# Kernel tuning notes

Measured on AMD Instinct MI355X. Metric: run time of the kernel, lower is better.

Reference implementation:

```python
import jax, jax.numpy as jnp
import numpy as np

B, T, D = 2, 2048, 2048
H, HD = 16, 128            # num_heads, head_dim = D // H
DVH = 2                    # dynamic_value_num_heads
NVK = 4                    # num_v_keys = int(sqrt(H))
TOPK = DVH * 2             # = 4 <= NVK


def setup_inputs() -> dict:
    key = jax.random.key(0)
    ks = jax.random.split(key, 12)
    s = jnp.float32(0.02)
    return {
        "x": jax.random.normal(ks[0], (B, T, D), jnp.float32),
        "Wq": jax.random.normal(ks[1], (D, D), jnp.float32) * s,
        "bq": jnp.zeros((D,), jnp.float32),
        "Wk": jax.random.normal(ks[2], (D, D), jnp.float32) * s,
        "bk": jnp.zeros((D,), jnp.float32),
        "Wvq": jax.random.normal(ks[3], (HD * DVH, D), jnp.float32) * s,
        "bvq": jnp.zeros((HD * DVH,), jnp.float32),
        "v_keys": jax.random.normal(ks[4], (DVH, NVK, HD), jnp.float32) * s,
        "v_embed": jax.random.normal(ks[5], (H, HD * H), jnp.float32) * s,
        "Wo": jax.random.normal(ks[6], (D, D), jnp.float32) * s,
        "bo": jnp.zeros((D,), jnp.float32),
    }


def reference(x, Wq, bq, Wk, bk, Wvq, bvq, v_keys, v_embed, Wo, bo):
    b, t, d = x.shape
    # q/k projections -> [b, H, t, HD]
    q = (x @ Wq.T + bq).reshape(b, t, H, HD).transpose(0, 2, 1, 3)
    k = (x @ Wk.T + bk).reshape(b, t, H, HD).transpose(0, 2, 1, 3)

    # --- compute_value_states ---
    vq = (x @ Wvq.T + bvq).reshape(b, t, DVH, HD)          # [b,t,h,n]
    sim = jnp.einsum('bthn,hkn->bthk', vq, v_keys)         # [b,t,DVH,NVK]
    _, idx = jax.lax.top_k(sim, TOPK)                      # [b,t,DVH,TOPK]
    ve = v_embed[idx]                                      # gather -> [b,t,DVH,TOPK,d]
    # einsum 'btd,bthkd->btd' == x * sum over (h,k)
    vs = x * ve.sum(axis=(2, 3))                           # [b,t,d]
    v = vs.reshape(b, t, H, HD).transpose(0, 2, 1, 3)      # [b,H,t,HD]

    # --- hand-rolled causal attention ---
    scores = jnp.einsum('bhqd,bhkd->bhqk', q, k) / np.float32(np.sqrt(HD))
    min_val = jnp.finfo(x.dtype).min
    mask = jnp.triu(jnp.full((t, t), min_val, dtype=x.dtype), 1)
    scores = scores + mask
    w = jax.nn.softmax(scores.astype(jnp.float32), axis=-1).astype(x.dtype)
    o = jnp.einsum('bhqk,bhkd->bhqd', w, v)                # [b,H,t,HD]
    o = o.transpose(0, 2, 1, 3).reshape(b, t, d)
    return o @ Wo.T + bo
```

## Files before the change

kernel.cpp:

```cpp
#include <hip/hip_runtime.h>
#include <hip/hip_bf16.h>

#define DEV __device__ __forceinline__

typedef __bf16 bf16x8 __attribute__((ext_vector_type(8)));
typedef __bf16 bf16x4 __attribute__((ext_vector_type(4)));
typedef float f32x4 __attribute__((ext_vector_type(4)));

static constexpr int kB = 2, kT = 2048, kD = 2048, kH = 16, kHD = 128;
static constexpr int kBT = kB * kT;

#if __has_builtin(__builtin_amdgcn_exp2f)
DEV float fast_exp2(float x) { return __builtin_amdgcn_exp2f(x); }
#else
DEV float fast_exp2(float x) { return exp2f(x); }
#endif

DEV unsigned short f2bf(float f) {
  union { __hip_bfloat16 h; unsigned short u; } cv;
  cv.h = __float2bfloat16(f);
  return cv.u;
}

DEV void gl_lds16(const void* g, void* l) {
  __builtin_amdgcn_global_load_lds(
      (const __attribute__((address_space(1))) unsigned int*)g,
      (__attribute__((address_space(3))) unsigned int*)l, 16, 0, 0);
}

#define MFMA(a, b, c) __builtin_amdgcn_mfma_f32_16x16x32_bf16(a, b, c, 0, 0, 0)

DEV int swz4(int row) { return (row ^ (row >> 2)) & 3; }

__global__ __launch_bounds__(256) void cvt4_kernel(
    const float* __restrict__ s0, const float* __restrict__ s1,
    const float* __restrict__ s2, const float* __restrict__ s3,
    unsigned short* __restrict__ d0, unsigned short* __restrict__ d1,
    unsigned short* __restrict__ d2, unsigned short* __restrict__ d3,
    int n0, int n1) {
  const int y = blockIdx.y;
  const float* s = y == 0 ? s0 : y == 1 ? s1 : y == 2 ? s2 : s3;
  unsigned short* d = y == 0 ? d0 : y == 1 ? d1 : y == 2 ? d2 : d3;
  const int n4 = y == 0 ? n0 : n1;
  int i = blockIdx.x * 256 + threadIdx.x;
  if (i >= n4) return;
  float4 v = ((const float4*)s)[i];
  ushort4 o;
  o.x = f2bf(v.x); o.y = f2bf(v.y); o.z = f2bf(v.z); o.w = f2bf(v.w);
  ((ushort4*)d)[i] = o;
}

__global__ __launch_bounds__(256) void make_vt_kernel(
    const float* __restrict__ x, const float* __restrict__ v_embed,
    unsigned short* __restrict__ vt) {
  __shared__ __align__(16) unsigned short sT[128 * 72];
  const int t0 = blockIdx.x * 64, h = blockIdx.y, b = blockIdx.z;
  const int tid = threadIdx.x;
  const int d4 = tid & 31, r8 = tid >> 5;
  const int dg = h * kHD + d4 * 4;
  float4 e0 = *(const float4*)(v_embed + dg);
  float4 e1 = *(const float4*)(v_embed + kD + dg);
  float4 e2 = *(const float4*)(v_embed + 2 * kD + dg);
  float4 e3 = *(const float4*)(v_embed + 3 * kD + dg);
  float4 c4;
  c4.x = 2.f * (e0.x + e1.x + e2.x + e3.x);
  c4.y = 2.f * (e0.y + e1.y + e2.y + e3.y);
  c4.z = 2.f * (e0.z + e1.z + e2.z + e3.z);
  c4.w = 2.f * (e0.w + e1.w + e2.w + e3.w);
#pragma unroll
  for (int it = 0; it < 8; it++) {
    const int t = r8 + it * 8;
    float4 v = *(const float4*)(x + (size_t)(b * kT + t0 + t) * kD + dg);
    sT[(d4 * 4 + 0) * 72 + t] = f2bf(v.x * c4.x);
    sT[(d4 * 4 + 1) * 72 + t] = f2bf(v.y * c4.y);
    sT[(d4 * 4 + 2) * 72 + t] = f2bf(v.z * c4.z);
    sT[(d4 * 4 + 3) * 72 + t] = f2bf(v.w * c4.w);
  }
  __syncthreads();
#pragma unroll
  for (int it = 0; it < 4; it++) {
    const int hd = (tid >> 3) + it * 32;
    const int tt = (tid & 7) * 8;
    bf16x8 vv = *(const bf16x8*)(sT + hd * 72 + tt);
    *(bf16x8*)(vt + ((size_t)((b * kH + h) * kHD + hd)) * kT + t0 + tt) = vv;
  }
}

template <bool BF16OUT, bool FUSED2>
__global__ __launch_bounds__(256, 4) void gemm_bt(
    const unsigned short* __restrict__ A, const unsigned short* __restrict__ B1,
    const unsigned short* __restrict__ B2, const float* __restrict__ bias1,
    const float* __restrict__ bias2, void* __restrict__ C1, void* __restrict__ C2,
    float scale1, float scale2) {
  constexpr int N = kD, K = kD;
  __shared__ __align__(16) unsigned short As[128 * 32], Bs[128 * 32];
  const unsigned short* Bm = (FUSED2 && blockIdx.z) ? B2 : B1;
  const float* bias = (FUSED2 && blockIdx.z) ? bias2 : bias1;
  void* Cout = (FUSED2 && blockIdx.z) ? C2 : C1;
  const float scale = (FUSED2 && blockIdx.z) ? scale2 : scale1;
  const int tid = threadIdx.x;
  const int lane = tid & 63, wave = tid >> 6;
  const int wr = wave >> 1, wc = wave & 1;
  const int m0 = blockIdx.y * 128, n0 = blockIdx.x * 128;
  const int frow = lane & 15, fc = lane >> 4;

  f32x4 acc[4][4];
  for (int i = 0; i < 4; i++)
    for (int j = 0; j < 4; j++)
      for (int r = 0; r < 4; r++) acc[i][j][r] = 0.f;

  const int r0 = tid >> 2, c0 = (tid & 3) ^ swz4(r0);
  const int p1 = tid + 256;
  const int r1 = p1 >> 2, c1 = (p1 & 3) ^ swz4(r1);

  const unsigned short* Ab = A + (size_t)m0 * K;
  const unsigned short* Bb = Bm + (size_t)n0 * K;

  for (int k0 = 0; k0 < K; k0 += 32) {
    __syncthreads();
    gl_lds16(Ab + (size_t)r0 * K + k0 + c0 * 8, As + tid * 8);
    gl_lds16(Ab + (size_t)r1 * K + k0 + c1 * 8, As + p1 * 8);
    gl_lds16(Bb + (size_t)r0 * K + k0 + c0 * 8, Bs + tid * 8);
    gl_lds16(Bb + (size_t)r1 * K + k0 + c1 * 8, Bs + p1 * 8);
    __syncthreads();
    bf16x8 af[4], bfr[4];
    for (int mi = 0; mi < 4; mi++) {
      int row = wr * 64 + mi * 16 + frow;
      af[mi] = *(const bf16x8*)(As + (row * 4 + (fc ^ swz4(row))) * 8);
    }
    for (int ni = 0; ni < 4; ni++) {
      int row = wc * 64 + ni * 16 + frow;
      bfr[ni] = *(const bf16x8*)(Bs + (row * 4 + (fc ^ swz4(row))) * 8);
    }
    for (int mi = 0; mi < 4; mi++)
      for (int ni = 0; ni < 4; ni++)
        acc[mi][ni] = MFMA(af[mi], bfr[ni], acc[mi][ni]);
  }
  for (int ni = 0; ni < 4; ni++) {
    const int n = n0 + wc * 64 + ni * 16 + frow;
    const float bs = bias[n];
    for (int mi = 0; mi < 4; mi++) {
      const int mb = m0 + wr * 64 + mi * 16 + fc * 4;
      for (int r = 0; r < 4; r++) {
        const float v = (acc[mi][ni][r] + bs) * scale;
        if (BF16OUT)
          ((unsigned short*)Cout)[(size_t)(mb + r) * N + n] = f2bf(v);
        else
          ((float*)Cout)[(size_t)(mb + r) * N + n] = v;
      }
    }
  }
}

__global__ __launch_bounds__(256, 2) void attn2_kernel(
    const unsigned short* __restrict__ Q, const unsigned short* __restrict__ Kg,
    const unsigned short* __restrict__ Vt, unsigned short* __restrict__ O) {
  __shared__ __align__(16) unsigned short sK[2][64 * 128];
  __shared__ __align__(16) unsigned short sV[2][64 * 128];
  const int tid = threadIdx.x, l = tid & 63, w = tid >> 6;
  const int g = l >> 4, q15 = l & 15;
  const int bid = blockIdx.x;
  const int xcd = bid & 7, rest = bid >> 3;
  const int gidx = xcd + 8 * (rest & 3);
  const int pi = rest >> 2;
  const int h = gidx & 15, b = gidx >> 4;

  for (int half = 0; half < 2; half++) {
    const int qt = half == 0 ? (31 - pi) : pi;
    const int q0 = qt * 64;
    const int nkb = qt + 1;
    const int q = q0 + w * 16 + q15;

    __syncthreads();
    for (int i = 0; i < 4; i++) {
      const int idx = tid + i * 256;
      const int key = idx >> 4, cc = (idx & 15) ^ (key & 15);
      gl_lds16(Kg + (size_t)(b * kT + key) * kD + h * kHD + cc * 8,
               &sK[0][idx * 8]);
    }
    for (int i = 0; i < 4; i++) {
      const int idx = tid + i * 256;
      const int hd = idx >> 3;
      const int cc = (idx & 7) ^ (hd & 7) ^ (((hd >> 3) & 1) << 2);
      gl_lds16(Vt + ((size_t)((b * kH + h) * kHD + hd)) * kT + cc * 8,
               &sV[0][idx * 8]);
    }

    bf16x8 qf[4];
    const unsigned short* Qrow = Q + (size_t)(b * kT + q) * kD + h * kHD;
#pragma unroll
    for (int kk = 0; kk < 4; kk++)
      qf[kk] = *(const bf16x8*)(Qrow + kk * 32 + g * 8);

    f32x4 oacc[8];
#pragma unroll
    for (int ni = 0; ni < 8; ni++)
      for (int r = 0; r < 4; r++) oacc[ni][r] = 0.f;
    float m_i = -1e30f, l_i = 0.f;

    for (int kb = 0; kb < nkb; kb++) {
      const int bb = kb & 1;
      __syncthreads();
      if (kb + 1 < nkb) {
        const int k0n = (kb + 1) * 64;
        const int nb = 1 - bb;
#pragma unroll
        for (int i = 0; i < 4; i++) {
          const int idx = tid + i * 256;
          const int key = idx >> 4, cc = (idx & 15) ^ (key & 15);
          gl_lds16(Kg + (size_t)(b * kT + k0n + key) * kD + h * kHD + cc * 8,
                   &sK[nb][idx * 8]);
        }
#pragma unroll
        for (int i = 0; i < 4; i++) {
          const int idx = tid + i * 256;
          const int hd = idx >> 3;
          const int cc = (idx & 7) ^ (hd & 7) ^ (((hd >> 3) & 1) << 2);
          gl_lds16(Vt + ((size_t)((b * kH + h) * kHD + hd)) * kT + k0n + cc * 8,
                   &sV[nb][idx * 8]);
        }
      }

      f32x4 st[4];
#pragma unroll
      for (int s = 0; s < 4; s++)
        for (int r = 0; r < 4; r++) st[s][r] = 0.f;
#pragma unroll
      for (int s = 0; s < 4; s++) {
        const int key = s * 16 + q15;
#pragma unroll
        for (int kk = 0; kk < 4; kk++) {
          bf16x8 kf = *(const bf16x8*)(
              &sK[bb][(key * 16 + ((kk * 4 + g) ^ (key & 15))) * 8]);
          st[s] = MFMA(kf, qf[kk], st[s]);
        }
      }
      if (kb == nkb - 1) {
        const int k0 = kb * 64;
#pragma unroll
        for (int s = 0; s < 4; s++)
          for (int r = 0; r < 4; r++)
            if (k0 + s * 16 + g * 4 + r > q) st[s][r] = -1e30f;
      }
      float mx = -1e30f;
#pragma unroll
      for (int s = 0; s < 4; s++)
        for (int r = 0; r < 4; r++) mx = fmaxf(mx, st[s][r]);
      mx = fmaxf(mx, __shfl_xor(mx, 16, 64));
      mx = fmaxf(mx, __shfl_xor(mx, 32, 64));
      const float mn = fmaxf(m_i, mx);
      const float alpha = fast_exp2(m_i - mn);
      float rs = 0.f;
      union { bf16x8 v; unsigned short u[8]; } pkv[2];
#pragma unroll
      for (int s = 0; s < 4; s++)
        for (int r = 0; r < 4; r++) {
          const float p = fast_exp2(st[s][r] - mn);
          rs += p;
          pkv[s >> 1].u[(s & 1) * 4 + r] = f2bf(p);
        }
      rs += __shfl_xor(rs, 16, 64);
      rs += __shfl_xor(rs, 32, 64);
      m_i = mn;
      l_i = l_i * alpha + rs;
#pragma unroll
      for (int ni = 0; ni < 8; ni++)
        for (int r = 0; r < 4; r++) oacc[ni][r] *= alpha;
#pragma unroll
      for (int ni = 0; ni < 8; ni++) {
        const int hd = ni * 16 + q15;
        const int hx = (hd & 7) ^ (((hd >> 3) & 1) << 2), base = hd * 8;
#pragma unroll
        for (int c = 0; c < 2; c++) {
          const int c4l = 8 * c + g;
          const int c4h = 8 * c + 4 + g;
          bf16x4 lo = *(const bf16x4*)(
              &sV[bb][(base + ((c4l >> 1) ^ hx)) * 8 + (c4l & 1) * 4]);
          bf16x4 hi = *(const bf16x4*)(
              &sV[bb][(base + ((c4h >> 1) ^ hx)) * 8 + (c4h & 1) * 4]);
          bf16x8 vf = __builtin_shufflevector(lo, hi, 0, 1, 2, 3, 4, 5, 6, 7);
          oacc[ni] = MFMA(vf, pkv[c].v, oacc[ni]);
        }
      }
    }
    const float inv = 1.f / l_i;
    unsigned short* Orow = O + (size_t)(b * kT + q) * kD + h * kHD;
#pragma unroll
    for (int ni = 0; ni < 8; ni++) {
      ushort4 o4;
      o4.x = f2bf(oacc[ni][0] * inv);
      o4.y = f2bf(oacc[ni][1] * inv);
      o4.z = f2bf(oacc[ni][2] * inv);
      o4.w = f2bf(oacc[ni][3] * inv);
      *(ushort4*)(Orow + ni * 16 + g * 4) = o4;
    }
  }
}

extern "C" void kernel_launch(void* const* d_in, const int* in_sizes, int n_in,
                              void* d_out, int out_size, void* d_ws, size_t ws_size,
                              hipStream_t stream) {
  const float* x       = (const float*)d_in[0];
  const float* Wq      = (const float*)d_in[1];
  const float* bq      = (const float*)d_in[2];
  const float* Wk      = (const float*)d_in[3];
  const float* bk      = (const float*)d_in[4];
  const float* v_embed = (const float*)d_in[8];
  const float* Wo      = (const float*)d_in[9];
  const float* bo      = (const float*)d_in[10];
  float* out = (float*)d_out;

  char* w = (char*)d_ws;
  unsigned short* xb  = (unsigned short*)w; w += (size_t)kBT * kD * 2;
  unsigned short* qb  = (unsigned short*)w; w += (size_t)kBT * kD * 2;
  unsigned short* kb  = (unsigned short*)w; w += (size_t)kBT * kD * 2;
  unsigned short* ob  = (unsigned short*)w; w += (size_t)kBT * kD * 2;
  unsigned short* vtb = (unsigned short*)w; w += (size_t)kBT * kD * 2;
  unsigned short* wqb = (unsigned short*)w; w += (size_t)kD * kD * 2;
  unsigned short* wkb = (unsigned short*)w; w += (size_t)kD * kD * 2;
  unsigned short* wob = (unsigned short*)w; w += (size_t)kD * kD * 2;

  cvt4_kernel<<<dim3(kBT * kD / 1024, 4), 256, 0, stream>>>(
      x, Wq, Wk, Wo, xb, wqb, wkb, wob, kBT * kD / 4, kD * kD / 4);
  make_vt_kernel<<<dim3(kT / 64, kH, kB), 256, 0, stream>>>(x, v_embed, vtb);

  const float scaleQ = 0.08838834764831845f * 1.4426950408889634f;
  gemm_bt<true, true><<<dim3(kD / 128, kBT / 128, 2), 256, 0, stream>>>(
      xb, wqb, wkb, bq, bk, qb, kb, scaleQ, 1.0f);

  attn2_kernel<<<dim3(512), 256, 0, stream>>>(qb, kb, vtb, ob);

  gemm_bt<false, false><<<dim3(kD / 128, kBT / 128, 1), 256, 0, stream>>>(
      ob, wob, nullptr, bo, nullptr, out, nullptr, 1.0f, 1.0f);
}
```

Before: 337.6 us.

## Fuse x conversion into V build, deepen GEMM K-tile, 128-row attention tiles

The x-to-bf16 conversion moves into make_vt_kernel, which already reads x, so x is no longer read twice. That kernel's LDS transpose also switches from a padded layout to an XOR-swizzled one. The GEMM K-step grows from 32 to 64, which halves the number of barriers per tile at the cost of twice the LDS. Attention blocks now own 128 query rows each, split as two 16-row groups per wave, so every K/V tile loaded into LDS is reused for twice as many queries. The cost is more registers per thread, with possible occupancy loss, and a different balance of causal work across blocks.

```diff
diff --git a/kernel.cpp b/kernel.cpp
--- a/kernel.cpp
+++ b/kernel.cpp
@@ -30,18 +30,15 @@
 
 #define MFMA(a, b, c) __builtin_amdgcn_mfma_f32_16x16x32_bf16(a, b, c, 0, 0, 0)
 
-DEV int swz4(int row) { return (row ^ (row >> 2)) & 3; }
-
-__global__ __launch_bounds__(256) void cvt4_kernel(
+DEV int swz8(int row) { return (row ^ (row >> 3)) & 7; }
+
+__global__ __launch_bounds__(256) void cvt3_kernel(
     const float* __restrict__ s0, const float* __restrict__ s1,
-    const float* __restrict__ s2, const float* __restrict__ s3,
-    unsigned short* __restrict__ d0, unsigned short* __restrict__ d1,
-    unsigned short* __restrict__ d2, unsigned short* __restrict__ d3,
-    int n0, int n1) {
+    const float* __restrict__ s2, unsigned short* __restrict__ d0,
+    unsigned short* __restrict__ d1, unsigned short* __restrict__ d2, int n4) {
   const int y = blockIdx.y;
-  const float* s = y == 0 ? s0 : y == 1 ? s1 : y == 2 ? s2 : s3;
-  unsigned short* d = y == 0 ? d0 : y == 1 ? d1 : y == 2 ? d2 : d3;
-  const int n4 = y == 0 ? n0 : n1;
+  const float* s = y == 0 ? s0 : y == 1 ? s1 : s2;
+  unsigned short* d = y == 0 ? d0 : y == 1 ? d1 : d2;
   int i = blockIdx.x * 256 + threadIdx.x;
   if (i >= n4) return;
   float4 v = ((const float4*)s)[i];
@@ -52,37 +49,47 @@
 
 __global__ __launch_bounds__(256) void make_vt_kernel(
     const float* __restrict__ x, const float* __restrict__ v_embed,
-    unsigned short* __restrict__ vt) {
-  __shared__ __align__(16) unsigned short sT[128 * 72];
+    unsigned short* __restrict__ vt, unsigned short* __restrict__ xb) {
+  __shared__ __align__(16) unsigned short sT[128 * 64];
   const int t0 = blockIdx.x * 64, h = blockIdx.y, b = blockIdx.z;
   const int tid = threadIdx.x;
-  const int d4 = tid & 31, r8 = tid >> 5;
+  const int d4 = tid & 31, tw = tid >> 5;
   const int dg = h * kHD + d4 * 4;
   float4 e0 = *(const float4*)(v_embed + dg);
   float4 e1 = *(const float4*)(v_embed + kD + dg);
   float4 e2 = *(const float4*)(v_embed + 2 * kD + dg);
   float4 e3 = *(const float4*)(v_embed + 3 * kD + dg);
-  float4 c4;
-  c4.x = 2.f * (e0.x + e1.x + e2.x + e3.x);
-  c4.y = 2.f * (e0.y + e1.y + e2.y + e3.y);
-  c4.z = 2.f * (e0.z + e1.z + e2.z + e3.z);
-  c4.w = 2.f * (e0.w + e1.w + e2.w + e3.w);
-#pragma unroll
-  for (int it = 0; it < 8; it++) {
-    const int t = r8 + it * 8;
-    float4 v = *(const float4*)(x + (size_t)(b * kT + t0 + t) * kD + dg);
-    sT[(d4 * 4 + 0) * 72 + t] = f2bf(v.x * c4.x);
-    sT[(d4 * 4 + 1) * 72 + t] = f2bf(v.y * c4.y);
-    sT[(d4 * 4 + 2) * 72 + t] = f2bf(v.z * c4.z);
-    sT[(d4 * 4 + 3) * 72 + t] = f2bf(v.w * c4.w);
+  float c4[4];
+  c4[0] = 2.f * (e0.x + e1.x + e2.x + e3.x);
+  c4[1] = 2.f * (e0.y + e1.y + e2.y + e3.y);
+  c4[2] = 2.f * (e0.z + e1.z + e2.z + e3.z);
+  c4[3] = 2.f * (e0.w + e1.w + e2.w + e3.w);
+  float4 v[8];
+#pragma unroll
+  for (int j = 0; j < 8; j++)
+    v[j] = *(const float4*)(x + (size_t)(b * kT + t0 + tw * 8 + j) * kD + dg);
+#pragma unroll
+  for (int j = 0; j < 8; j++) {
+    ushort4 o;
+    o.x = f2bf(v[j].x); o.y = f2bf(v[j].y); o.z = f2bf(v[j].z); o.w = f2bf(v[j].w);
+    *(ushort4*)(xb + (size_t)(b * kT + t0 + tw * 8 + j) * kD + dg) = o;
+  }
+#pragma unroll
+  for (int c = 0; c < 4; c++) {
+    const int hd = d4 * 4 + c;
+    union { bf16x8 v8; unsigned short u[8]; } w8;
+#pragma unroll
+    for (int j = 0; j < 8; j++)
+      w8.u[j] = f2bf(((const float*)&v[j])[c] * c4[c]);
+    *(bf16x8*)(&sT[hd * 64 + (tw ^ (hd & 7)) * 8]) = w8.v8;
   }
   __syncthreads();
 #pragma unroll
   for (int it = 0; it < 4; it++) {
     const int hd = (tid >> 3) + it * 32;
-    const int tt = (tid & 7) * 8;
-    bf16x8 vv = *(const bf16x8*)(sT + hd * 72 + tt);
-    *(bf16x8*)(vt + ((size_t)((b * kH + h) * kHD + hd)) * kT + t0 + tt) = vv;
+    const int rc = tid & 7;
+    bf16x8 vv = *(const bf16x8*)(&sT[hd * 64 + (rc ^ (hd & 7)) * 8]);
+    *(bf16x8*)(vt + ((size_t)((b * kH + h) * kHD + hd)) * kT + t0 + rc * 8) = vv;
   }
 }
 
@@ -93,7 +100,7 @@
     const float* __restrict__ bias2, void* __restrict__ C1, void* __restrict__ C2,
     float scale1, float scale2) {
   constexpr int N = kD, K = kD;
-  __shared__ __align__(16) unsigned short As[128 * 32], Bs[128 * 32];
+  __shared__ __align__(16) unsigned short As[128 * 64], Bs[128 * 64];
   const unsigned short* Bm = (FUSED2 && blockIdx.z) ? B2 : B1;
   const float* bias = (FUSED2 && blockIdx.z) ? bias2 : bias1;
   void* Cout = (FUSED2 && blockIdx.z) ? C2 : C1;
@@ -109,32 +116,43 @@
     for (int j = 0; j < 4; j++)
       for (int r = 0; r < 4; r++) acc[i][j][r] = 0.f;
 
-  const int r0 = tid >> 2, c0 = (tid & 3) ^ swz4(r0);
-  const int p1 = tid + 256;
-  const int r1 = p1 >> 2, c1 = (p1 & 3) ^ swz4(r1);
-
   const unsigned short* Ab = A + (size_t)m0 * K;
   const unsigned short* Bb = Bm + (size_t)n0 * K;
 
-  for (int k0 = 0; k0 < K; k0 += 32) {
+  for (int k0 = 0; k0 < K; k0 += 64) {
     __syncthreads();
-    gl_lds16(Ab + (size_t)r0 * K + k0 + c0 * 8, As + tid * 8);
-    gl_lds16(Ab + (size_t)r1 * K + k0 + c1 * 8, As + p1 * 8);
-    gl_lds16(Bb + (size_t)r0 * K + k0 + c0 * 8, Bs + tid * 8);
-    gl_lds16(Bb + (size_t)r1 * K + k0 + c1 * 8, Bs + p1 * 8);
+#pragma unroll
+    for (int i = 0; i < 8; i++) {
+      const int idx = tid + i * 256;
+      const int row = idx >> 3, dc = (idx & 7) ^ swz8(row);
+      gl_lds16(Ab + (size_t)row * K + k0 + dc * 8, As + idx * 8);
+    }
+#pragma unroll
+    for (int i = 0; i < 8; i++) {
+      const int idx = tid + i * 256;
+      const int row = idx >> 3, dc = (idx & 7) ^ swz8(row);
+      gl_lds16(Bb + (size_t)row * K + k0 + dc * 8, Bs + idx * 8);
+    }
     __syncthreads();
-    bf16x8 af[4], bfr[4];
-    for (int mi = 0; mi < 4; mi++) {
-      int row = wr * 64 + mi * 16 + frow;
-      af[mi] = *(const bf16x8*)(As + (row * 4 + (fc ^ swz4(row))) * 8);
-    }
-    for (int ni = 0; ni < 4; ni++) {
-      int row = wc * 64 + ni * 16 + frow;
-      bfr[ni] = *(const bf16x8*)(Bs + (row * 4 + (fc ^ swz4(row))) * 8);
-    }
-    for (int mi = 0; mi < 4; mi++)
-      for (int ni = 0; ni < 4; ni++)
-        acc[mi][ni] = MFMA(af[mi], bfr[ni], acc[mi][ni]);
+#pragma unroll
+    for (int ks = 0; ks < 2; ks++) {
+      bf16x8 af[4], bfr[4];
+#pragma unroll
+      for (int mi = 0; mi < 4; mi++) {
+        const int row = wr * 64 + mi * 16 + frow;
+        af[mi] = *(const bf16x8*)(As + (row * 8 + ((ks * 4 + fc) ^ swz8(row))) * 8);
+      }
+#pragma unroll
+      for (int ni = 0; ni < 4; ni++) {
+        const int row = wc * 64 + ni * 16 + frow;
+        bfr[ni] = *(const bf16x8*)(Bs + (row * 8 + ((ks * 4 + fc) ^ swz8(row))) * 8);
+      }
+#pragma unroll
+      for (int mi = 0; mi < 4; mi++)
+#pragma unroll
+        for (int ni = 0; ni < 4; ni++)
+          acc[mi][ni] = MFMA(af[mi], bfr[ni], acc[mi][ni]);
+    }
   }
   for (int ni = 0; ni < 4; ni++) {
     const int n = n0 + wc * 64 + ni * 16 + frow;
@@ -152,7 +170,25 @@
   }
 }
 
-__global__ __launch_bounds__(256, 2) void attn2_kernel(
+DEV void stage_kv(const unsigned short* __restrict__ Kg,
+                  const unsigned short* __restrict__ Vt, unsigned short* dK,
+                  unsigned short* dV, int tid, int b, int h, int k0) {
+#pragma unroll
+  for (int i = 0; i < 4; i++) {
+    const int idx = tid + i * 256;
+    const int key = idx >> 4, cc = (idx & 15) ^ (key & 15);
+    gl_lds16(Kg + (size_t)(b * kT + k0 + key) * kD + h * kHD + cc * 8, dK + idx * 8);
+  }
+#pragma unroll
+  for (int i = 0; i < 4; i++) {
+    const int idx = tid + i * 256;
+    const int hd = idx >> 3;
+    const int cc = (idx & 7) ^ (hd & 7) ^ (((hd >> 3) & 1) << 2);
+    gl_lds16(Vt + ((size_t)((b * kH + h) * kHD + hd)) * kT + k0 + cc * 8, dV + idx * 8);
+  }
+}
+
+__global__ __launch_bounds__(256, 2) void attn3_kernel(
     const unsigned short* __restrict__ Q, const unsigned short* __restrict__ Kg,
     const unsigned short* __restrict__ Vt, unsigned short* __restrict__ O) {
   __shared__ __align__(16) unsigned short sK[2][64 * 128];
@@ -160,138 +196,118 @@
   const int tid = threadIdx.x, l = tid & 63, w = tid >> 6;
   const int g = l >> 4, q15 = l & 15;
   const int bid = blockIdx.x;
-  const int xcd = bid & 7, rest = bid >> 3;
-  const int gidx = xcd + 8 * (rest & 3);
-  const int pi = rest >> 2;
+  const int pair = bid >> 1, j = pair >> 5;
+  const int qt = (bid & 1) ? j : (15 - j);
+  const int gidx = pair & 31;
   const int h = gidx & 15, b = gidx >> 4;
-
-  for (int half = 0; half < 2; half++) {
-    const int qt = half == 0 ? (31 - pi) : pi;
-    const int q0 = qt * 64;
-    const int nkb = qt + 1;
-    const int q = q0 + w * 16 + q15;
-
+  const int q0 = qt * 128;
+  const int nkb = 2 * qt + 2;
+  const int qA = q0 + w * 32 + q15;
+
+  stage_kv(Kg, Vt, &sK[0][0], &sV[0][0], tid, b, h, 0);
+
+  bf16x8 qf[2][4];
+#pragma unroll
+  for (int g2 = 0; g2 < 2; g2++) {
+    const unsigned short* Qrow = Q + (size_t)(b * kT + qA + 16 * g2) * kD + h * kHD;
+#pragma unroll
+    for (int kk = 0; kk < 4; kk++)
+      qf[g2][kk] = *(const bf16x8*)(Qrow + kk * 32 + g * 8);
+  }
+
+  f32x4 oacc[2][8];
+#pragma unroll
+  for (int g2 = 0; g2 < 2; g2++)
+    for (int ni = 0; ni < 8; ni++)
+      for (int r = 0; r < 4; r++) oacc[g2][ni][r] = 0.f;
+  float m_i[2] = {-1e30f, -1e30f}, l_i[2] = {0.f, 0.f};
+
+  for (int kb = 0; kb < nkb; kb++) {
+    const int bb = kb & 1;
     __syncthreads();
-    for (int i = 0; i < 4; i++) {
-      const int idx = tid + i * 256;
-      const int key = idx >> 4, cc = (idx & 15) ^ (key & 15);
-      gl_lds16(Kg + (size_t)(b * kT + key) * kD + h * kHD + cc * 8,
-               &sK[0][idx * 8]);
-    }
-    for (int i = 0; i < 4; i++) {
-      const int idx = tid + i * 256;
-      const int hd = idx >> 3;
-      const int cc = (idx & 7) ^ (hd & 7) ^ (((hd >> 3) & 1) << 2);
-      gl_lds16(Vt + ((size_t)((b * kH + h) * kHD + hd)) * kT + cc * 8,
-               &sV[0][idx * 8]);
-    }
-
-    bf16x8 qf[4];
-    const unsigned short* Qrow = Q + (size_t)(b * kT + q) * kD + h * kHD;
-#pragma unroll
-    for (int kk = 0; kk < 4; kk++)
-      qf[kk] = *(const bf16x8*)(Qrow + kk * 32 + g * 8);
-
-    f32x4 oacc[8];
-#pragma unroll
-    for (int ni = 0; ni < 8; ni++)
-      for (int r = 0; r < 4; r++) oacc[ni][r] = 0.f;
-    float m_i = -1e30f, l_i = 0.f;
-
-    for (int kb = 0; kb < nkb; kb++) {
-      const int bb = kb & 1;
-      __syncthreads();
-      if (kb + 1 < nkb) {
-        const int k0n = (kb + 1) * 64;
-        const int nb = 1 - bb;
-#pragma unroll
-        for (int i = 0; i < 4; i++) {
-          const int idx = tid + i * 256;
-          const int key = idx >> 4, cc = (idx & 15) ^ (key & 15);
-          gl_lds16(Kg + (size_t)(b * kT + k0n + key) * kD + h * kHD + cc * 8,
-                   &sK[nb][idx * 8]);
-        }
-#pragma unroll
-        for (int i = 0; i < 4; i++) {
-          const int idx = tid + i * 256;
-          const int hd = idx >> 3;
-          const int cc = (idx & 7) ^ (hd & 7) ^ (((hd >> 3) & 1) << 2);
-          gl_lds16(Vt + ((size_t)((b * kH + h) * kHD + hd)) * kT + k0n + cc * 8,
-                   &sV[nb][idx * 8]);
-        }
-      }
-
-      f32x4 st[4];
-#pragma unroll
+    if (kb + 1 < nkb)
+      stage_kv(Kg, Vt, &sK[1 - bb][0], &sV[1 - bb][0], tid, b, h, (kb + 1) * 64);
+
+    f32x4 st[2][4];
+#pragma unroll
+    for (int g2 = 0; g2 < 2; g2++)
       for (int s = 0; s < 4; s++)
-        for (int r = 0; r < 4; r++) st[s][r] = 0.f;
-#pragma unroll
-      for (int s = 0; s < 4; s++) {
-        const int key = s * 16 + q15;
-#pragma unroll
-        for (int kk = 0; kk < 4; kk++) {
-          bf16x8 kf = *(const bf16x8*)(
-              &sK[bb][(key * 16 + ((kk * 4 + g) ^ (key & 15))) * 8]);
-          st[s] = MFMA(kf, qf[kk], st[s]);
-        }
-      }
-      if (kb == nkb - 1) {
-        const int k0 = kb * 64;
-#pragma unroll
+        for (int r = 0; r < 4; r++) st[g2][s][r] = 0.f;
+#pragma unroll
+    for (int s = 0; s < 4; s++) {
+      const int key = s * 16 + q15;
+#pragma unroll
+      for (int kk = 0; kk < 4; kk++) {
+        bf16x8 kf = *(const bf16x8*)(
+            &sK[bb][(key * 16 + ((kk * 4 + g) ^ (key & 15))) * 8]);
+        st[0][s] = MFMA(kf, qf[0][kk], st[0][s]);
+        st[1][s] = MFMA(kf, qf[1][kk], st[1][s]);
+      }
+    }
+    if (kb >= nkb - 2) {
+      const int kbase = kb * 64;
+#pragma unroll
+      for (int g2 = 0; g2 < 2; g2++)
         for (int s = 0; s < 4; s++)
           for (int r = 0; r < 4; r++)
-            if (k0 + s * 16 + g * 4 + r > q) st[s][r] = -1e30f;
-      }
+            if (kbase + s * 16 + g * 4 + r > qA + 16 * g2) st[g2][s][r] = -1e30f;
+    }
+    union { bf16x8 v; unsigned short u[8]; } pkv[2][2];
+#pragma unroll
+    for (int g2 = 0; g2 < 2; g2++) {
       float mx = -1e30f;
 #pragma unroll
       for (int s = 0; s < 4; s++)
-        for (int r = 0; r < 4; r++) mx = fmaxf(mx, st[s][r]);
+        for (int r = 0; r < 4; r++) mx = fmaxf(mx, st[g2][s][r]);
       mx = fmaxf(mx, __shfl_xor(mx, 16, 64));
       mx = fmaxf(mx, __shfl_xor(mx, 32, 64));
-      const float mn = fmaxf(m_i, mx);
-      const float alpha = fast_exp2(m_i - mn);
+      const float mn = fmaxf(m_i[g2], mx);
+      const float alpha = fast_exp2(m_i[g2] - mn);
       float rs = 0.f;
-      union { bf16x8 v; unsigned short u[8]; } pkv[2];
 #pragma unroll
       for (int s = 0; s < 4; s++)
         for (int r = 0; r < 4; r++) {
-          const float p = fast_exp2(st[s][r] - mn);
+          const float p = fast_exp2(st[g2][s][r] - mn);
           rs += p;
-          pkv[s >> 1].u[(s & 1) * 4 + r] = f2bf(p);
+          pkv[g2][s >> 1].u[(s & 1) * 4 + r] = f2bf(p);
         }
       rs += __shfl_xor(rs, 16, 64);
       rs += __shfl_xor(rs, 32, 64);
-      m_i = mn;
-      l_i = l_i * alpha + rs;
+      m_i[g2] = mn;
+      l_i[g2] = l_i[g2] * alpha + rs;
 #pragma unroll
       for (int ni = 0; ni < 8; ni++)
-        for (int r = 0; r < 4; r++) oacc[ni][r] *= alpha;
-#pragma unroll
-      for (int ni = 0; ni < 8; ni++) {
-        const int hd = ni * 16 + q15;
-        const int hx = (hd & 7) ^ (((hd >> 3) & 1) << 2), base = hd * 8;
-#pragma unroll
-        for (int c = 0; c < 2; c++) {
-          const int c4l = 8 * c + g;
-          const int c4h = 8 * c + 4 + g;
-          bf16x4 lo = *(const bf16x4*)(
-              &sV[bb][(base + ((c4l >> 1) ^ hx)) * 8 + (c4l & 1) * 4]);
-          bf16x4 hi = *(const bf16x4*)(
-              &sV[bb][(base + ((c4h >> 1) ^ hx)) * 8 + (c4h & 1) * 4]);
-          bf16x8 vf = __builtin_shufflevector(lo, hi, 0, 1, 2, 3, 4, 5, 6, 7);
-          oacc[ni] = MFMA(vf, pkv[c].v, oacc[ni]);
-        }
-      }
-    }
-    const float inv = 1.f / l_i;
-    unsigned short* Orow = O + (size_t)(b * kT + q) * kD + h * kHD;
+        for (int r = 0; r < 4; r++) oacc[g2][ni][r] *= alpha;
+    }
+#pragma unroll
+    for (int ni = 0; ni < 8; ni++) {
+      const int hd = ni * 16 + q15;
+      const int hx = (hd & 7) ^ (((hd >> 3) & 1) << 2), base = hd * 8;
+#pragma unroll
+      for (int c = 0; c < 2; c++) {
+        const int c4l = 8 * c + g;
+        const int c4h = 8 * c + 4 + g;
+        bf16x4 lo = *(const bf16x4*)(
+            &sV[bb][(base + ((c4l >> 1) ^ hx)) * 8 + (c4l & 1) * 4]);
+        bf16x4 hi = *(const bf16x4*)(
+            &sV[bb][(base + ((c4h >> 1) ^ hx)) * 8 + (c4h & 1) * 4]);
+        bf16x8 vf = __builtin_shufflevector(lo, hi, 0, 1, 2, 3, 4, 5, 6, 7);
+        oacc[0][ni] = MFMA(vf, pkv[0][c].v, oacc[0][ni]);
+        oacc[1][ni] = MFMA(vf, pkv[1][c].v, oacc[1][ni]);
+      }
+    }
+  }
+#pragma unroll
+  for (int g2 = 0; g2 < 2; g2++) {
+    const float inv = 1.f / l_i[g2];
+    unsigned short* Orow = O + (size_t)(b * kT + qA + 16 * g2) * kD + h * kHD;
 #pragma unroll
     for (int ni = 0; ni < 8; ni++) {
       ushort4 o4;
-      o4.x = f2bf(oacc[ni][0] * inv);
-      o4.y = f2bf(oacc[ni][1] * inv);
-      o4.z = f2bf(oacc[ni][2] * inv);
-      o4.w = f2bf(oacc[ni][3] * inv);
+      o4.x = f2bf(oacc[g2][ni][0] * inv);
+      o4.y = f2bf(oacc[g2][ni][1] * inv);
+      o4.z = f2bf(oacc[g2][ni][2] * inv);
+      o4.w = f2bf(oacc[g2][ni][3] * inv);
       *(ushort4*)(Orow + ni * 16 + g * 4) = o4;
     }
   }
@@ -320,15 +336,15 @@
   unsigned short* wkb = (unsigned short*)w; w += (size_t)kD * kD * 2;
   unsigned short* wob = (unsigned short*)w; w += (size_t)kD * kD * 2;
 
-  cvt4_kernel<<<dim3(kBT * kD / 1024, 4), 256, 0, stream>>>(
-      x, Wq, Wk, Wo, xb, wqb, wkb, wob, kBT * kD / 4, kD * kD / 4);
-  make_vt_kernel<<<dim3(kT / 64, kH, kB), 256, 0, stream>>>(x, v_embed, vtb);
+  make_vt_kernel<<<dim3(kT / 64, kH, kB), 256, 0, stream>>>(x, v_embed, vtb, xb);
+  cvt3_kernel<<<dim3(kD * kD / 1024, 3), 256, 0, stream>>>(
+      Wq, Wk, Wo, wqb, wkb, wob, kD * kD / 4);
 
   const float scaleQ = 0.08838834764831845f * 1.4426950408889634f;
   gemm_bt<true, true><<<dim3(kD / 128, kBT / 128, 2), 256, 0, stream>>>(
       xb, wqb, wkb, bq, bk, qb, kb, scaleQ, 1.0f);
 
-  attn2_kernel<<<dim3(512), 256, 0, stream>>>(qb, kb, vtb, ob);
+  attn3_kernel<<<dim3(512), 256, 0, stream>>>(qb, kb, vtb, ob);
 
   gemm_bt<false, false><<<dim3(kD / 128, kBT / 128, 1), 256, 0, stream>>>(
       ob, wob, nullptr, bo, nullptr, out, nullptr, 1.0f, 1.0f);
```

After: 460.8 us. 1.36x slower.
